# Performance work log

Hardware: AMD Instinct MI355X
Metric: run time of the kernel (lower is better)

## Reference

```python
import jax, jax.numpy as jnp
from jax import lax
import numpy as np

# Module hyperparameters (init_kwargs)
NITERS = 10
NROWS, NCOLS = 16, 16
NSUP = NROWS * NCOLS
COMPACT = 10.0
CONST = 100.0
NCONV = 10  # stage1_nconv; also nfeat of imfeat and shifter_size
B, H, W = 2, 512, 512

DN = ('NCHW', 'OIHW', 'NCHW')


def conv2d(x, w, b=None):
    y = lax.conv_general_dilated(x, w, (1, 1), 'SAME', dimension_numbers=DN)
    return y if b is None else y + b[None, :, None, None]


def blockmean(x):
    # adaptive_avg_pool2d to (NROWS, NCOLS); H,W chosen divisible -> exact block mean
    Bz, C, Hx, Wx = x.shape
    return x.reshape(Bz, C, NROWS, Hx // NROWS, NCOLS, Wx // NCOLS).mean((3, 5))


def box3(x):
    # 3x3 all-ones depthwise conv with zero padding (the "shifter" conv)
    C = x.shape[1]
    k = jnp.ones((C, 1, 3, 3), x.dtype)
    return lax.conv_general_dilated(x, k, (1, 1), 'SAME', feature_group_count=C,
                                    dimension_numbers=DN)


def setup_inputs() -> dict:
    key = jax.random.key(0)
    ks = jax.random.split(key, 7)
    s = 0.15  # ~He init for 3x3 convs with ~10 channels; keeps activations O(1)
    return {
        'X': jax.random.normal(ks[0], (B, 3, H, W), jnp.float32),
        'w0': jax.random.normal(ks[1], (NCONV, 3, 3, 3), jnp.float32) * s,
        'b0': jax.random.normal(ks[2], (NCONV,), jnp.float32) * s,
        'ws_mid': jax.random.normal(ks[3], (NCONV - 2, NCONV, NCONV, 3, 3), jnp.float32) * s,
        'bs_mid': jax.random.normal(ks[4], (NCONV - 2, NCONV), jnp.float32) * s,
        'wf': jax.random.normal(ks[5], (NCONV - 5, NCONV, 3, 3), jnp.float32) * s,
        'bf': jax.random.normal(ks[6], (NCONV - 5,), jnp.float32) * s,
    }


def _forward(X, w0, b0, ws_mid, bs_mid, wf, bf):
    Bz, _, Hx, Wx = X.shape
    h = jax.nn.relu(conv2d(X, w0, b0))

    def layer(hc, wb):
        w, b = wb
        return jax.nn.relu(conv2d(hc, w, b)), None

    h, _ = lax.scan(layer, h, (ws_mid, bs_mid))
    s1 = conv2d(h, wf, bf)  # B x (NCONV-5) x H x W

    # ---- imfeat = [stage1, X, Xgrid, Ygrid] -> B x NCONV x H x W ----
    Yg, Xg = jnp.meshgrid(jnp.arange(Hx, dtype=X.dtype), jnp.arange(Wx, dtype=X.dtype),
                          indexing='ij')
    imfeat = jnp.concatenate([
        s1, X,
        jnp.broadcast_to(Xg, (Bz, 1, Hx, Wx)),
        jnp.broadcast_to(Yg, (Bz, 1, Hx, Wx)),
    ], axis=1)
    C = imfeat.shape[1]

    # ckern: ones, except spatial (last two) channels weighted by compactness scale
    ck = jnp.ones((C,), imfeat.dtype).at[-2:].set(
        jnp.asarray(COMPACT / np.sqrt(Hx * Wx / NSUP), imfeat.dtype))

    # pixel -> parent superpixel indices (nearest-neighbor upsample of coarse grid)
    Yc = jnp.arange(Hx) * NROWS // Hx  # (H,)
    Xc = jnp.arange(Wx) * NCOLS // Wx  # (W,)
    shifts = [(dr, dc) for dr in (-1, 0, 1) for dc in (-1, 0, 1)]
    Y1 = jnp.stack([jnp.clip(Yc + dr, 0, NROWS - 1) for dr, _ in shifts])[:, :, None]  # (9,H,1)
    X1 = jnp.stack([jnp.clip(Xc + dc, 0, NCOLS - 1) for _, dc in shifts])[:, None, :]  # (9,1,W)

    def affinity_fn(cent):
        cup = cent[:, :, Y1, X1]
        d = (imfeat[:, :, None] - cup) * ck[None, :, None, None, None]
        return jnp.exp(-(d * d).mean(1) / CONST)

    def centroids_fn(aff):
        # sum over the 9 shifts commutes with block-mean and the shared 3x3 box conv
        asum = aff.sum(1, keepdims=True)
        num = box3(blockmean(imfeat * asum))  # B x C x NROWS x NCOLS
        den = box3(blockmean(asum))
        return num / den

    cent0 = blockmean(imfeat)
    aff0 = affinity_fn(cent0)

    @jax.checkpoint
    def step(carry, _):
        cent, _a = carry
        aff = affinity_fn(cent)
        return (centroids_fn(aff), aff), None

    (cent, aff), _ = lax.scan(step, (cent0, aff0), None, length=NITERS)
    # returned affinity corresponds to centroids before the last update (as in torch)
    return cent, aff


def reference(X, w0, b0, ws_mid, bs_mid, wf, bf):
    return _forward(X, w0, b0, ws_mid, bs_mid, wf, bf)
```

## Files before the change

kernel.cpp:

```cpp
#include <hip/hip_runtime.h>

#define HH 512
#define WW 512
#define BB 2
#define CKXY 0.3125f
#define HW (HH*WW)

typedef short bf16x8 __attribute__((ext_vector_type(8)));
typedef float f32x4  __attribute__((ext_vector_type(4)));

__device__ __forceinline__ unsigned short f2bf(float f) {
  unsigned u = __float_as_uint(f);
  u += 0x7FFF + ((u >> 16) & 1);
  return (unsigned short)(u >> 16);
}
__device__ __forceinline__ unsigned pack2(float lo, float hi) {
  return (unsigned)f2bf(lo) | ((unsigned)f2bf(hi) << 16);
}

template<int CIN, bool BF16IN>
__global__ __launch_bounds__(512) void conv_mfma_u(const void* __restrict__ in,
    const float* __restrict__ w, const float* __restrict__ bias,
    unsigned* __restrict__ outu) {
  const int bx = blockIdx.x, by = blockIdx.y, b = blockIdx.z;
  const int tid = threadIdx.x;
  const int gy0 = by * 32, gx0 = bx * 32;
  __shared__ unsigned short sT[34 * 34 * 16];

  const int lane = tid & 63;
  const int g = lane >> 4;
  const int co = lane & 15;
  bf16x8 Bf[5];
  #pragma unroll
  for (int P = 0; P < 5; ++P) {
    #pragma unroll
    for (int j = 0; j < 8; ++j) {
      const int tap = 2 * P + (g >> 1);
      const int ci = ((g & 1) << 3) + j;
      unsigned short v = 0;
      if (co < 10 && ci < CIN && tap < 9)
        v = f2bf(w[(co * CIN + ci) * 9 + tap]);
      Bf[P][j] = (short)v;
    }
  }
  const float bs = (co < 10) ? bias[co] : 0.f;

  for (int p = tid; p < 34 * 34; p += 512) {
    const int ly = p / 34, lx = p - ly * 34;
    const int gy = gy0 + ly - 1, gx = gx0 + lx - 1;
    const bool ok = ((unsigned)gy < HH) && ((unsigned)gx < WW);
    const int pix = gy * WW + gx;
    unsigned u[8];
    if (BF16IN) {
      const unsigned* pp = (const unsigned*)in + (size_t)b * 5 * HW + pix;
      #pragma unroll
      for (int c2 = 0; c2 < 8; ++c2)
        u[c2] = (c2 < (CIN + 1) / 2 && ok) ? pp[c2 * HW] : 0u;
    } else {
      const float* pp = (const float*)in + (size_t)b * CIN * HW + pix;
      #pragma unroll
      for (int c2 = 0; c2 < 8; ++c2) {
        float f0 = (2 * c2 < CIN && ok) ? pp[(2 * c2) * HW] : 0.f;
        float f1 = (2 * c2 + 1 < CIN && ok) ? pp[(2 * c2 + 1) * HW] : 0.f;
        u[c2] = pack2(f0, f1);
      }
    }
    uint4* dst = reinterpret_cast<uint4*>(&sT[p * 16]);
    dst[0] = make_uint4(u[0], u[1], u[2], u[3]);
    dst[1] = make_uint4(u[4], u[5], u[6], u[7]);
  }
  __syncthreads();

  const int wave = tid >> 6;
  unsigned* ob = outu + (size_t)b * 5 * HW;
  for (int i = 0; i < 8; ++i) {
    const int t = wave * 8 + i;
    const int py = t >> 1;
    const int pxb = (t & 1) << 4;
    f32x4 acc = {bs, bs, bs, bs};
    #pragma unroll
    for (int P = 0; P < 5; ++P) {
      int tap = 2 * P + (g >> 1);
      if (tap > 8) tap = 8;
      const int dy = tap / 3 - 1, dx = tap % 3 - 1;
      const int m = lane & 15;
      const int addr = ((py + 1 + dy) * 34 + (pxb + m + 1 + dx)) * 16 + ((g & 1) << 3);
      bf16x8 a = *reinterpret_cast<const bf16x8*>(&sT[addr]);
      acc = __builtin_amdgcn_mfma_f32_16x16x32_bf16(a, Bf[P], acc, 0, 0, 0);
    }
    float o0 = fmaxf(acc[0], 0.f), o1 = fmaxf(acc[1], 0.f);
    float o2 = fmaxf(acc[2], 0.f), o3 = fmaxf(acc[3], 0.f);
    const float q0 = __shfl_xor(o0, 1), q1 = __shfl_xor(o1, 1);
    const float q2 = __shfl_xor(o2, 1), q3 = __shfl_xor(o3, 1);
    if (!(co & 1) && co < 10) {
      const int y = gy0 + py;
      const int x = gx0 + pxb + (g << 2);
      uint4 st;
      st.x = pack2(o0, q0); st.y = pack2(o1, q1);
      st.z = pack2(o2, q2); st.w = pack2(o3, q3);
      *reinterpret_cast<uint4*>(&ob[(co >> 1) * HW + y * WW + x]) = st;
    }
  }
}

__global__ __launch_bounds__(512) void conv_final_mfma(const unsigned* __restrict__ in,
    const float* __restrict__ w, const float* __restrict__ bias,
    const float* __restrict__ X, unsigned* __restrict__ imfeat,
    float* __restrict__ cent0) {
  const int bx = blockIdx.x, by = blockIdx.y, b = blockIdx.z;
  const int tid = threadIdx.x;
  const int gy0 = by * 32, gx0 = bx * 32;
  __shared__ unsigned short sT[34 * 34 * 16];
  __shared__ float sC[8][5];
  __shared__ float sX[8][3];

  const int lane = tid & 63;
  const int g = lane >> 4;
  const int co = lane & 15;
  bf16x8 Bf[5];
  #pragma unroll
  for (int P = 0; P < 5; ++P) {
    #pragma unroll
    for (int j = 0; j < 8; ++j) {
      const int tap = 2 * P + (g >> 1);
      const int ci = ((g & 1) << 3) + j;
      unsigned short v = 0;
      if (co < 5 && ci < 10 && tap < 9)
        v = f2bf(w[(co * 10 + ci) * 9 + tap]);
      Bf[P][j] = (short)v;
    }
  }
  const float bs = (co < 5) ? bias[co] : 0.f;

  for (int p = tid; p < 34 * 34; p += 512) {
    const int ly = p / 34, lx = p - ly * 34;
    const int gy = gy0 + ly - 1, gx = gx0 + lx - 1;
    const bool ok = ((unsigned)gy < HH) && ((unsigned)gx < WW);
    const unsigned* pp = in + (size_t)b * 5 * HW + gy * WW + gx;
    unsigned u[5];
    #pragma unroll
    for (int c2 = 0; c2 < 5; ++c2) u[c2] = ok ? pp[c2 * HW] : 0u;
    uint4* dst = reinterpret_cast<uint4*>(&sT[p * 16]);
    dst[0] = make_uint4(u[0], u[1], u[2], u[3]);
    dst[1] = make_uint4(u[4], 0u, 0u, 0u);
  }
  __syncthreads();

  const int wave = tid >> 6;
  unsigned* ob = imfeat + (size_t)b * 5 * HW;
  const float* Xb = X + (size_t)b * 3 * HW;
  float cSum = 0.f;
  for (int i = 0; i < 8; ++i) {
    const int t = wave * 8 + i;
    const int py = t >> 1;
    const int pxb = (t & 1) << 4;
    f32x4 acc = {bs, bs, bs, bs};
    #pragma unroll
    for (int P = 0; P < 5; ++P) {
      int tap = 2 * P + (g >> 1);
      if (tap > 8) tap = 8;
      const int dy = tap / 3 - 1, dx = tap % 3 - 1;
      const int m = lane & 15;
      const int addr = ((py + 1 + dy) * 34 + (pxb + m + 1 + dx)) * 16 + ((g & 1) << 3);
      bf16x8 a = *reinterpret_cast<const bf16x8*>(&sT[addr]);
      acc = __builtin_amdgcn_mfma_f32_16x16x32_bf16(a, Bf[P], acc, 0, 0, 0);
    }
    const int y = gy0 + py;
    const int x = gx0 + pxb + (g << 2);
    const float q0 = __shfl_xor(acc[0], 1), q1 = __shfl_xor(acc[1], 1);
    const float q2 = __shfl_xor(acc[2], 1), q3 = __shfl_xor(acc[3], 1);
    if (co == 0 || co == 2) {
      uint4 st;
      st.x = pack2(acc[0], q0); st.y = pack2(acc[1], q1);
      st.z = pack2(acc[2], q2); st.w = pack2(acc[3], q3);
      *reinterpret_cast<uint4*>(&ob[(co >> 1) * HW + y * WW + x]) = st;
    } else if (co == 4) {
      float4 xv = *reinterpret_cast<const float4*>(&Xb[y * WW + x]);
      uint4 st;
      st.x = pack2(acc[0], xv.x); st.y = pack2(acc[1], xv.y);
      st.z = pack2(acc[2], xv.z); st.w = pack2(acc[3], xv.w);
      *reinterpret_cast<uint4*>(&ob[2 * HW + y * WW + x]) = st;
    }
    cSum += acc[0] + acc[1] + acc[2] + acc[3];
  }
  cSum += __shfl_xor(cSum, 16);
  cSum += __shfl_xor(cSum, 32);
  if (lane < 5) sC[wave][lane] = cSum;

  float xs[3] = {0.f, 0.f, 0.f};
  for (int p = tid; p < 1024; p += 512) {
    const int y = gy0 + (p >> 5), x = gx0 + (p & 31);
    const int pix = y * WW + x;
    float x0 = Xb[pix];
    float x1 = Xb[HW + pix];
    float x2 = Xb[2 * HW + pix];
    xs[0] += x0; xs[1] += x1; xs[2] += x2;
    ob[3 * HW + pix] = pack2(x1, x2);
    ob[4 * HW + pix] = pack2((float)x * CKXY, (float)y * CKXY);
  }
  #pragma unroll
  for (int off = 32; off; off >>= 1) {
    #pragma unroll
    for (int c = 0; c < 3; ++c) xs[c] += __shfl_down(xs[c], off);
  }
  if (lane == 0) {
    #pragma unroll
    for (int c = 0; c < 3; ++c) sX[wave][c] = xs[c];
  }
  __syncthreads();
  if (tid < 5) {
    float s = 0.f;
    #pragma unroll
    for (int wv = 0; wv < 8; ++wv) s += sC[wv][tid];
    cent0[((b * 10 + tid) * 16 + by) * 16 + bx] = s * (1.0f / 1024.0f);
  }
  if (tid >= 64 && tid < 67) {
    const int c = tid - 64;
    float s = 0.f;
    #pragma unroll
    for (int wv = 0; wv < 8; ++wv) s += sX[wv][c];
    cent0[((b * 10 + 5 + c) * 16 + by) * 16 + bx] = s * (1.0f / 1024.0f);
  }
  if (tid == 128) cent0[((b * 10 + 8) * 16 + by) * 16 + bx] = ((float)gx0 + 15.5f) * CKXY;
  if (tid == 129) cent0[((b * 10 + 9) * 16 + by) * 16 + bx] = ((float)gy0 + 15.5f) * CKXY;
}

__global__ __launch_bounds__(256) void iter2(const unsigned* __restrict__ imfeat,
    const float* __restrict__ centIn, const float* __restrict__ numP,
    const float* __restrict__ denP, float* __restrict__ numO,
    float* __restrict__ denO, float* __restrict__ affO) {
  const int cx = blockIdx.x, cy = blockIdx.y, b = blockIdx.z;
  const int tid = threadIdx.x;
  __shared__ float sc[9][10];
  __shared__ float nb[9][11];
  if (centIn) {
    if (tid < 90) {
      int s = tid / 10, ch = tid - s * 10;
      int dr = s / 3 - 1, dc = s % 3 - 1;
      int r = min(max(cy + dr, 0), 15), c = min(max(cx + dc, 0), 15);
      sc[s][ch] = centIn[((b * 10 + ch) * 16 + r) * 16 + c];
    }
    __syncthreads();
  } else {
    if (tid < 99) {
      int s = tid / 11, j = tid - s * 11;
      int dr = s / 3 - 1, dc = s % 3 - 1;
      int r = min(max(cy + dr, 0), 15), c = min(max(cx + dc, 0), 15);
      float a = 0.f;
      #pragma unroll
      for (int rr = -1; rr <= 1; ++rr)
        #pragma unroll
        for (int cc = -1; cc <= 1; ++cc) {
          int R = r + rr, C = c + cc;
          if ((unsigned)R < 16u && (unsigned)C < 16u)
            a += (j < 10) ? numP[((b * 10 + j) * 16 + R) * 16 + C]
                          : denP[(b * 16 + R) * 16 + C];
        }
      nb[s][j] = a;
    }
    __syncthreads();
    if (tid < 90) {
      int s = tid / 10, ch = tid - s * 10;
      sc[s][ch] = nb[s][ch] / nb[s][10];
    }
    __syncthreads();
  }

  float accN[10];
  #pragma unroll
  for (int ch = 0; ch < 10; ++ch) accN[ch] = 0.f;
  float accD = 0.f;
  const int col = tid & 31, row0 = tid >> 5;
  for (int p = 0; p < 4; ++p) {
    const int y = cy * 32 + row0 + p * 8;
    const int x = cx * 32 + col;
    const unsigned* fb = imfeat + (size_t)b * 5 * HW + y * WW + x;
    float f[10];
    #pragma unroll
    for (int c2 = 0; c2 < 5; ++c2) {
      unsigned u = fb[c2 * HW];
      f[2 * c2]     = __uint_as_float(u << 16);
      f[2 * c2 + 1] = __uint_as_float(u & 0xFFFF0000u);
    }
    float asum = 0.f;
    #pragma unroll
    for (int s = 0; s < 9; ++s) {
      float ss = 0.f;
      #pragma unroll
      for (int ch = 0; ch < 10; ++ch) { float d = f[ch] - sc[s][ch]; ss = fmaf(d, d, ss); }
      float a = __expf(-ss * (1.0f / 1000.0f));
      asum += a;
      if (affO) affO[((b * 9 + s) * HH + y) * WW + x] = a;
    }
    accD += asum;
    #pragma unroll
    for (int ch = 0; ch < 10; ++ch) accN[ch] = fmaf(f[ch], asum, accN[ch]);
  }
  #pragma unroll
  for (int off = 32; off; off >>= 1) {
    accD += __shfl_down(accD, off);
    #pragma unroll
    for (int ch = 0; ch < 10; ++ch) accN[ch] += __shfl_down(accN[ch], off);
  }
  __shared__ float sPart[4][11];
  const int wave = tid >> 6, lane = tid & 63;
  if (lane == 0) {
    #pragma unroll
    for (int ch = 0; ch < 10; ++ch) sPart[wave][ch] = accN[ch];
    sPart[wave][10] = accD;
  }
  __syncthreads();
  if (tid < 11) {
    float s = sPart[0][tid] + sPart[1][tid] + sPart[2][tid] + sPart[3][tid];
    if (tid < 10) numO[((b * 10 + tid) * 16 + cy) * 16 + cx] = s;
    else denO[(b * 16 + cy) * 16 + cx] = s;
  }
}

__global__ __launch_bounds__(256) void cent_final(const float* __restrict__ num_bs,
    const float* __restrict__ den_bs, float* __restrict__ out_cent) {
  const int b = blockIdx.x;
  const int tid = threadIdx.x;
  const int cy = tid >> 4, cx = tid & 15;
  float den = 0.f;
  #pragma unroll
  for (int dr = -1; dr <= 1; ++dr)
    #pragma unroll
    for (int dc = -1; dc <= 1; ++dc) {
      int r = cy + dr, c = cx + dc;
      if ((unsigned)r < 16 && (unsigned)c < 16) den += den_bs[(b * 16 + r) * 16 + c];
    }
  #pragma unroll
  for (int ch = 0; ch < 10; ++ch) {
    float num = 0.f;
    #pragma unroll
    for (int dr = -1; dr <= 1; ++dr)
      #pragma unroll
      for (int dc = -1; dc <= 1; ++dc) {
        int r = cy + dr, c = cx + dc;
        if ((unsigned)r < 16 && (unsigned)c < 16)
          num += num_bs[((b * 10 + ch) * 16 + r) * 16 + c];
      }
    float invck = (ch >= 8) ? (1.0f / CKXY) : 1.0f;
    out_cent[((b * 10 + ch) * 16 + cy) * 16 + cx] = (num / den) * invck;
  }
}

extern "C" void kernel_launch(void* const* d_in, const int* in_sizes, int n_in,
                              void* d_out, int out_size, void* d_ws, size_t ws_size,
                              hipStream_t stream) {
  const float* X      = (const float*)d_in[0];
  const float* w0     = (const float*)d_in[1];
  const float* b0     = (const float*)d_in[2];
  const float* ws_mid = (const float*)d_in[3];
  const float* bs_mid = (const float*)d_in[4];
  const float* wf     = (const float*)d_in[5];
  const float* bf     = (const float*)d_in[6];
  float* out = (float*)d_out;

  const size_t uplane = (size_t)BB * 5 * HW;
  unsigned* uA     = (unsigned*)d_ws;
  unsigned* uB     = uA + uplane;
  unsigned* imfeat = uB + uplane;
  float* num0      = (float*)(imfeat + uplane);
  float* den0      = num0 + BB * 10 * 256;
  float* num1      = den0 + BB * 256;
  float* den1      = num1 + BB * 10 * 256;
  float* centA     = den1 + BB * 256;

  dim3 cgrid(16, 16, BB);
  conv_mfma_u<3, false><<<cgrid, 512, 0, stream>>>(X, w0, b0, uA);
  const unsigned* cur = uA;
  unsigned* nxt = uB;
  for (int l = 0; l < 8; ++l) {
    conv_mfma_u<10, true><<<cgrid, 512, 0, stream>>>(cur, ws_mid + l * 900, bs_mid + l * 10, nxt);
    const unsigned* t = cur; cur = nxt; nxt = (unsigned*)t;
  }
  conv_final_mfma<<<cgrid, 512, 0, stream>>>(cur, wf, bf, X, imfeat, centA);

  float* aff_out = out + BB * 10 * 256;
  float* nums[2] = {num0, num1};
  float* dens[2] = {den0, den1};
  for (int k = 0; k < 10; ++k) {
    iter2<<<cgrid, 256, 0, stream>>>(imfeat,
        (k == 0) ? centA : nullptr,
        (k == 0) ? nullptr : nums[(k - 1) & 1],
        (k == 0) ? nullptr : dens[(k - 1) & 1],
        nums[k & 1], dens[k & 1],
        (k == 9) ? aff_out : nullptr);
  }
  cent_final<<<dim3(BB), 256, 0, stream>>>(nums[1], dens[1], out);
}
```

Before: 260.1 us.

## Store conv activations pixel-interleaved and read MFMA operands directly from global

Intermediate CNN activations change from planar bf16-pair channel planes to a pixel-major layout with 8 packed words (16 bf16 channels) per pixel. The middle and final convolutions then load each MFMA A-operand as one 16-byte global read per tap instead of staging a haloed tile in shared memory, and the middle layers use a flat 2048-block grid of 256 threads. The aim is to remove the LDS staging, the barrier and the strided multi-plane gathers. In exchange, intermediate buffers grow (16 padded channels versus 10), halo pixels are re-read through cache, and outputs go out as scattered 4-byte stores.

Measured after the change: 365.9 us. 1.41x slower.

```diff
diff --git a/kernel.cpp b/kernel.cpp
--- a/kernel.cpp
+++ b/kernel.cpp
@@ -5,6 +5,7 @@
 #define BB 2
 #define CKXY 0.3125f
 #define HW (HH*WW)
+#define PXPLANE (HH*WW*8)
 
 typedef short bf16x8 __attribute__((ext_vector_type(8)));
 typedef float f32x4  __attribute__((ext_vector_type(4)));
@@ -18,10 +19,9 @@
   return (unsigned)f2bf(lo) | ((unsigned)f2bf(hi) << 16);
 }
 
-template<int CIN, bool BF16IN>
-__global__ __launch_bounds__(512) void conv_mfma_u(const void* __restrict__ in,
+__global__ __launch_bounds__(512) void conv1_px(const float* __restrict__ X,
     const float* __restrict__ w, const float* __restrict__ bias,
-    unsigned* __restrict__ outu) {
+    unsigned* __restrict__ outp) {
   const int bx = blockIdx.x, by = blockIdx.y, b = blockIdx.z;
   const int tid = threadIdx.x;
   const int gy0 = by * 32, gx0 = bx * 32;
@@ -38,8 +38,8 @@
       const int tap = 2 * P + (g >> 1);
       const int ci = ((g & 1) << 3) + j;
       unsigned short v = 0;
-      if (co < 10 && ci < CIN && tap < 9)
-        v = f2bf(w[(co * CIN + ci) * 9 + tap]);
+      if (co < 10 && ci < 3 && tap < 9)
+        v = f2bf(w[(co * 3 + ci) * 9 + tap]);
       Bf[P][j] = (short)v;
     }
   }
@@ -49,30 +49,20 @@
     const int ly = p / 34, lx = p - ly * 34;
     const int gy = gy0 + ly - 1, gx = gx0 + lx - 1;
     const bool ok = ((unsigned)gy < HH) && ((unsigned)gx < WW);
-    const int pix = gy * WW + gx;
-    unsigned u[8];
-    if (BF16IN) {
-      const unsigned* pp = (const unsigned*)in + (size_t)b * 5 * HW + pix;
-      #pragma unroll
-      for (int c2 = 0; c2 < 8; ++c2)
-        u[c2] = (c2 < (CIN + 1) / 2 && ok) ? pp[c2 * HW] : 0u;
-    } else {
-      const float* pp = (const float*)in + (size_t)b * CIN * HW + pix;
-      #pragma unroll
-      for (int c2 = 0; c2 < 8; ++c2) {
-        float f0 = (2 * c2 < CIN && ok) ? pp[(2 * c2) * HW] : 0.f;
-        float f1 = (2 * c2 + 1 < CIN && ok) ? pp[(2 * c2 + 1) * HW] : 0.f;
-        u[c2] = pack2(f0, f1);
-      }
+    const float* pp = X + (size_t)b * 3 * HW + gy * WW + gx;
+    unsigned u0 = 0, u1 = 0;
+    if (ok) {
+      u0 = pack2(pp[0], pp[HW]);
+      u1 = pack2(pp[2 * HW], 0.f);
     }
     uint4* dst = reinterpret_cast<uint4*>(&sT[p * 16]);
-    dst[0] = make_uint4(u[0], u[1], u[2], u[3]);
-    dst[1] = make_uint4(u[4], u[5], u[6], u[7]);
+    dst[0] = make_uint4(u0, u1, 0u, 0u);
+    dst[1] = make_uint4(0u, 0u, 0u, 0u);
   }
   __syncthreads();
 
   const int wave = tid >> 6;
-  unsigned* ob = outu + (size_t)b * 5 * HW;
+  unsigned* ob = outp + (size_t)b * PXPLANE;
   for (int i = 0; i < 8; ++i) {
     const int t = wave * 8 + i;
     const int py = t >> 1;
@@ -92,25 +82,86 @@
     float o2 = fmaxf(acc[2], 0.f), o3 = fmaxf(acc[3], 0.f);
     const float q0 = __shfl_xor(o0, 1), q1 = __shfl_xor(o1, 1);
     const float q2 = __shfl_xor(o2, 1), q3 = __shfl_xor(o3, 1);
-    if (!(co & 1) && co < 10) {
+    if (!(co & 1)) {
       const int y = gy0 + py;
-      const int x = gx0 + pxb + (g << 2);
-      uint4 st;
-      st.x = pack2(o0, q0); st.y = pack2(o1, q1);
-      st.z = pack2(o2, q2); st.w = pack2(o3, q3);
-      *reinterpret_cast<uint4*>(&ob[(co >> 1) * HW + y * WW + x]) = st;
-    }
-  }
-}
-
-__global__ __launch_bounds__(512) void conv_final_mfma(const unsigned* __restrict__ in,
+      const int xb = gx0 + pxb + (g << 2);
+      ob[((y << 9) + xb + 0) * 8 + (co >> 1)] = pack2(o0, q0);
+      ob[((y << 9) + xb + 1) * 8 + (co >> 1)] = pack2(o1, q1);
+      ob[((y << 9) + xb + 2) * 8 + (co >> 1)] = pack2(o2, q2);
+      ob[((y << 9) + xb + 3) * 8 + (co >> 1)] = pack2(o3, q3);
+    }
+  }
+}
+
+__global__ __launch_bounds__(256) void conv_mid_px(const unsigned* __restrict__ in,
+    const float* __restrict__ w, const float* __restrict__ bias,
+    unsigned* __restrict__ out) {
+  const int tid = threadIdx.x;
+  const int lane = tid & 63;
+  const int wv = tid >> 6;
+  const int g = lane >> 4;
+  const int co = lane & 15;
+  const int m = lane & 15;
+
+  bf16x8 Bf[5];
+  #pragma unroll
+  for (int P = 0; P < 5; ++P) {
+    #pragma unroll
+    for (int j = 0; j < 8; ++j) {
+      const int tap = 2 * P + (g >> 1);
+      const int ci = ((g & 1) << 3) + j;
+      unsigned short v = 0;
+      if (co < 10 && ci < 10 && tap < 9)
+        v = f2bf(w[(co * 10 + ci) * 9 + tap]);
+      Bf[P][j] = (short)v;
+    }
+  }
+  const float bs = (co < 10) ? bias[co] : 0.f;
+
+  const int base_t = blockIdx.x * 16 + wv * 4;
+  #pragma unroll
+  for (int i = 0; i < 4; ++i) {
+    const int t = base_t + i;
+    const int b = t >> 14;
+    const int rem = t & 16383;
+    const int py = rem >> 5;
+    const int pxb = (rem & 31) << 4;
+    const unsigned* ib = in + (size_t)b * PXPLANE;
+    f32x4 acc = {bs, bs, bs, bs};
+    #pragma unroll
+    for (int P = 0; P < 5; ++P) {
+      int tap = 2 * P + (g >> 1);
+      if (tap > 8) tap = 8;
+      const int dy = tap / 3 - 1, dx = tap % 3 - 1;
+      const int yy = py + dy;
+      const int xx = pxb + m + dx;
+      bf16x8 a = {};
+      if (((unsigned)yy < (unsigned)HH) && ((unsigned)xx < (unsigned)WW))
+        a = *reinterpret_cast<const bf16x8*>(&ib[(((yy << 9) + xx) << 3) + ((g & 1) << 2)]);
+      acc = __builtin_amdgcn_mfma_f32_16x16x32_bf16(a, Bf[P], acc, 0, 0, 0);
+    }
+    float o0 = fmaxf(acc[0], 0.f), o1 = fmaxf(acc[1], 0.f);
+    float o2 = fmaxf(acc[2], 0.f), o3 = fmaxf(acc[3], 0.f);
+    const float q0 = __shfl_xor(o0, 1), q1 = __shfl_xor(o1, 1);
+    const float q2 = __shfl_xor(o2, 1), q3 = __shfl_xor(o3, 1);
+    if (!(co & 1)) {
+      unsigned* ob = out + (size_t)b * PXPLANE;
+      const int xb = pxb + (g << 2);
+      ob[((py << 9) + xb + 0) * 8 + (co >> 1)] = pack2(o0, q0);
+      ob[((py << 9) + xb + 1) * 8 + (co >> 1)] = pack2(o1, q1);
+      ob[((py << 9) + xb + 2) * 8 + (co >> 1)] = pack2(o2, q2);
+      ob[((py << 9) + xb + 3) * 8 + (co >> 1)] = pack2(o3, q3);
+    }
+  }
+}
+
+__global__ __launch_bounds__(512) void conv_final_px(const unsigned* __restrict__ in,
     const float* __restrict__ w, const float* __restrict__ bias,
     const float* __restrict__ X, unsigned* __restrict__ imfeat,
     float* __restrict__ cent0) {
   const int bx = blockIdx.x, by = blockIdx.y, b = blockIdx.z;
   const int tid = threadIdx.x;
   const int gy0 = by * 32, gx0 = bx * 32;
-  __shared__ unsigned short sT[34 * 34 * 16];
   __shared__ float sC[8][5];
   __shared__ float sX[8][3];
 
@@ -132,21 +183,8 @@
   }
   const float bs = (co < 5) ? bias[co] : 0.f;
 
-  for (int p = tid; p < 34 * 34; p += 512) {
-    const int ly = p / 34, lx = p - ly * 34;
-    const int gy = gy0 + ly - 1, gx = gx0 + lx - 1;
-    const bool ok = ((unsigned)gy < HH) && ((unsigned)gx < WW);
-    const unsigned* pp = in + (size_t)b * 5 * HW + gy * WW + gx;
-    unsigned u[5];
-    #pragma unroll
-    for (int c2 = 0; c2 < 5; ++c2) u[c2] = ok ? pp[c2 * HW] : 0u;
-    uint4* dst = reinterpret_cast<uint4*>(&sT[p * 16]);
-    dst[0] = make_uint4(u[0], u[1], u[2], u[3]);
-    dst[1] = make_uint4(u[4], 0u, 0u, 0u);
-  }
-  __syncthreads();
-
   const int wave = tid >> 6;
+  const unsigned* ib = in + (size_t)b * PXPLANE;
   unsigned* ob = imfeat + (size_t)b * 5 * HW;
   const float* Xb = X + (size_t)b * 3 * HW;
   float cSum = 0.f;
@@ -160,9 +198,11 @@
       int tap = 2 * P + (g >> 1);
       if (tap > 8) tap = 8;
       const int dy = tap / 3 - 1, dx = tap % 3 - 1;
-      const int m = lane & 15;
-      const int addr = ((py + 1 + dy) * 34 + (pxb + m + 1 + dx)) * 16 + ((g & 1) << 3);
-      bf16x8 a = *reinterpret_cast<const bf16x8*>(&sT[addr]);
+      const int yy = gy0 + py + dy;
+      const int xx = gx0 + pxb + (lane & 15) + dx;
+      bf16x8 a = {};
+      if (((unsigned)yy < (unsigned)HH) && ((unsigned)xx < (unsigned)WW))
+        a = *reinterpret_cast<const bf16x8*>(&ib[(((yy << 9) + xx) << 3) + ((g & 1) << 2)]);
       acc = __builtin_amdgcn_mfma_f32_16x16x32_bf16(a, Bf[P], acc, 0, 0, 0);
     }
     const int y = gy0 + py;
@@ -358,25 +398,24 @@
   const float* bf     = (const float*)d_in[6];
   float* out = (float*)d_out;
 
-  const size_t uplane = (size_t)BB * 5 * HW;
-  unsigned* uA     = (unsigned*)d_ws;
-  unsigned* uB     = uA + uplane;
-  unsigned* imfeat = uB + uplane;
-  float* num0      = (float*)(imfeat + uplane);
+  unsigned* pxA    = (unsigned*)d_ws;
+  unsigned* pxB    = pxA + (size_t)BB * PXPLANE;
+  unsigned* imfeat = pxB + (size_t)BB * PXPLANE;
+  float* num0      = (float*)(imfeat + (size_t)BB * 5 * HW);
   float* den0      = num0 + BB * 10 * 256;
   float* num1      = den0 + BB * 256;
   float* den1      = num1 + BB * 10 * 256;
   float* centA     = den1 + BB * 256;
 
   dim3 cgrid(16, 16, BB);
-  conv_mfma_u<3, false><<<cgrid, 512, 0, stream>>>(X, w0, b0, uA);
-  const unsigned* cur = uA;
-  unsigned* nxt = uB;
+  conv1_px<<<cgrid, 512, 0, stream>>>(X, w0, b0, pxA);
+  const unsigned* cur = pxA;
+  unsigned* nxt = pxB;
   for (int l = 0; l < 8; ++l) {
-    conv_mfma_u<10, true><<<cgrid, 512, 0, stream>>>(cur, ws_mid + l * 900, bs_mid + l * 10, nxt);
+    conv_mid_px<<<dim3(2048), 256, 0, stream>>>(cur, ws_mid + l * 900, bs_mid + l * 10, nxt);
     const unsigned* t = cur; cur = nxt; nxt = (unsigned*)t;
   }
-  conv_final_mfma<<<cgrid, 512, 0, stream>>>(cur, wf, bf, X, imfeat, centA);
+  conv_final_px<<<cgrid, 512, 0, stream>>>(cur, wf, bf, X, imfeat, centA);
 
   float* aff_out = out + BB * 10 * 256;
   float* nums[2] = {num0, num1};
```

## Fuse four mid conv layers per kernel with halo tiles in shared memory

Applied to the files above, without the earlier changes.

Replaces eight separate mid-layer conv launches with two launches that each run four conv+relu layers on a 40x40 halo tile held in LDS, ping-ponging between two shared buffers. The goal is to remove the global-memory round trips and launch overhead between layers. The cost is redundant halo recomputation (40x40 shrinking to 32x32 per block), a large LDS footprint that limits occupancy to one 1024-thread block per CU, and a block-wide barrier after every layer.

Result: slower. 287.8 us (+10.7%).

```diff
diff --git a/kernel.cpp b/kernel.cpp
--- a/kernel.cpp
+++ b/kernel.cpp
@@ -100,6 +100,109 @@
       st.z = pack2(o2, q2); st.w = pack2(o3, q3);
       *reinterpret_cast<uint4*>(&ob[(co >> 1) * HW + y * WW + x]) = st;
     }
+  }
+}
+
+__global__ __launch_bounds__(1024) void conv_mid4(const unsigned* __restrict__ in,
+    const float* __restrict__ ws, const float* __restrict__ bs_all,
+    unsigned* __restrict__ out, int lbase) {
+  const int bx = blockIdx.x, by = blockIdx.y, b = blockIdx.z;
+  const int tid = threadIdx.x;
+  const int gy0 = by * 32, gx0 = bx * 32;
+  __shared__ unsigned short sL[2 * 25600];
+
+  const int lane = tid & 63;
+  const int wv = tid >> 6;
+  const int g = lane >> 4;
+  const int co = lane & 15;
+  const int m = lane & 15;
+
+  for (int p = tid; p < 1600; p += 1024) {
+    const int ly = p / 40, lx = p - ly * 40;
+    const int gy = gy0 + ly - 4, gx = gx0 + lx - 4;
+    const bool ok = ((unsigned)gy < HH) && ((unsigned)gx < WW);
+    const unsigned* pp = in + (size_t)b * 5 * HW + gy * WW + gx;
+    unsigned u[5];
+    #pragma unroll
+    for (int c2 = 0; c2 < 5; ++c2) u[c2] = ok ? pp[c2 * HW] : 0u;
+    uint4* dst = reinterpret_cast<uint4*>(&sL[p * 16]);
+    dst[0] = make_uint4(u[0], u[1], u[2], u[3]);
+    dst[1] = make_uint4(u[4], 0u, 0u, 0u);
+  }
+  __syncthreads();
+
+  #pragma unroll
+  for (int l = 0; l < 4; ++l) {
+    const int w_in = 40 - 2 * l;
+    const int w_out = w_in - 2;
+    const unsigned short* bin = &sL[(l & 1) * 25600];
+    unsigned short* bout = &sL[((l & 1) ^ 1) * 25600];
+    const float* w = ws + (size_t)(lbase + l) * 900;
+    const float* bias = bs_all + (size_t)(lbase + l) * 10;
+
+    bf16x8 Bf[5];
+    #pragma unroll
+    for (int P = 0; P < 5; ++P) {
+      #pragma unroll
+      for (int j = 0; j < 8; ++j) {
+        const int tap = 2 * P + (g >> 1);
+        const int ci = ((g & 1) << 3) + j;
+        unsigned short v = 0;
+        if (co < 10 && ci < 10 && tap < 9)
+          v = f2bf(w[(co * 10 + ci) * 9 + tap]);
+        Bf[P][j] = (short)v;
+      }
+    }
+    const float bsv = (co < 10) ? bias[co] : 0.f;
+
+    const int nseg = (w_out + 15) >> 4;
+    const int T = w_out * nseg;
+    for (int t = wv; t < T; t += 16) {
+      const int r = t / nseg, s = t - r * nseg;
+      f32x4 acc = {bsv, bsv, bsv, bsv};
+      #pragma unroll
+      for (int P = 0; P < 5; ++P) {
+        int tap = 2 * P + (g >> 1);
+        if (tap > 8) tap = 8;
+        const int dy = tap / 3 - 1, dx = tap % 3 - 1;
+        const int row = r + 1 + dy;
+        int col = (s << 4) + m + 1 + dx;
+        col = min(col, w_in - 1);
+        bf16x8 a = *reinterpret_cast<const bf16x8*>(
+            &bin[(row * 40 + col) * 16 + ((g & 1) << 3)]);
+        acc = __builtin_amdgcn_mfma_f32_16x16x32_bf16(a, Bf[P], acc, 0, 0, 0);
+      }
+      float o0 = fmaxf(acc[0], 0.f), o1 = fmaxf(acc[1], 0.f);
+      float o2 = fmaxf(acc[2], 0.f), o3 = fmaxf(acc[3], 0.f);
+      const float q0 = __shfl_xor(o0, 1), q1 = __shfl_xor(o1, 1);
+      const float q2 = __shfl_xor(o2, 1), q3 = __shfl_xor(o3, 1);
+      if (!(co & 1)) {
+        const int xb = (s << 4) + (g << 2);
+        unsigned vals[4] = {pack2(o0, q0), pack2(o1, q1),
+                            pack2(o2, q2), pack2(o3, q3)};
+        #pragma unroll
+        for (int k = 0; k < 4; ++k) {
+          const int x = xb + k;
+          if (x < w_out)
+            *reinterpret_cast<unsigned*>(&bout[(r * 40 + x) * 16 + co]) = vals[k];
+        }
+      }
+    }
+    __syncthreads();
+  }
+
+  const unsigned short* fin = &sL[0];
+  unsigned* ob = out + (size_t)b * 5 * HW;
+  {
+    const int r = tid >> 5, c = tid & 31;
+    const uint4 v4 = *reinterpret_cast<const uint4*>(&fin[(r * 40 + c) * 16]);
+    const unsigned v5 = *reinterpret_cast<const unsigned*>(&fin[(r * 40 + c) * 16 + 8]);
+    const int pix = (gy0 + r) * WW + gx0 + c;
+    ob[0 * HW + pix] = v4.x;
+    ob[1 * HW + pix] = v4.y;
+    ob[2 * HW + pix] = v4.z;
+    ob[3 * HW + pix] = v4.w;
+    ob[4 * HW + pix] = v5;
   }
 }
 
@@ -370,13 +473,9 @@
 
   dim3 cgrid(16, 16, BB);
   conv_mfma_u<3, false><<<cgrid, 512, 0, stream>>>(X, w0, b0, uA);
-  const unsigned* cur = uA;
-  unsigned* nxt = uB;
-  for (int l = 0; l < 8; ++l) {
-    conv_mfma_u<10, true><<<cgrid, 512, 0, stream>>>(cur, ws_mid + l * 900, bs_mid + l * 10, nxt);
-    const unsigned* t = cur; cur = nxt; nxt = (unsigned*)t;
-  }
-  conv_final_mfma<<<cgrid, 512, 0, stream>>>(cur, wf, bf, X, imfeat, centA);
+  conv_mid4<<<cgrid, 1024, 0, stream>>>(uA, ws_mid, bs_mid, uB, 0);
+  conv_mid4<<<cgrid, 1024, 0, stream>>>(uB, ws_mid, bs_mid, uA, 4);
+  conv_final_mfma<<<cgrid, 512, 0, stream>>>(uA, wf, bf, X, imfeat, centA);
 
   float* aff_out = out + BB * 10 * 256;
   float* nums[2] = {num0, num1};
```
